# Performance work log

Measured on AMD Instinct MI355X. Metric: run time of the kernel, lower is better.

## Reference

```python
import jax, jax.numpy as jnp
import numpy as np

T, A = 768, 24          # tokens, dense atoms per token
S, Q, K = 576, 32, 128  # subsets, queries per subset, keys per subset
C, H, DH, L = 128, 4, 32, 3  # c_query, heads, head dim, transformer blocks
PAIR, PTC, FF = 16, 384, 256


def _ln(x, s, b):
    m = jnp.mean(x, axis=-1, keepdims=True)
    v = jnp.var(x, axis=-1, keepdims=True)
    return (x - m) * jax.lax.rsqrt(v + 1e-5) * s + b


def _convert(idxs, mask, arr):
    # atom_layout.convertV2: flatten the two layout axes, gather, apply mask
    flat = arr.reshape(-1, arr.shape[-1])
    return flat[idxs] * mask[..., None].astype(arr.dtype)


def setup_inputs() -> dict:
    key = jax.random.key(0)
    ks = jax.random.split(key, 32)
    sc = 0.02
    inp = {
        'queries_mask': jax.random.randint(ks[0], (S, Q), 0, 2, dtype=jnp.int32),
        'pred_dense_atom_mask': jax.random.randint(ks[1], (T, A), 0, 2, dtype=jnp.int32),
        'acat_atoms_to_q_gather_idxs': jax.random.randint(ks[2], (S, Q), 0, T * A, dtype=jnp.int32),
        'acat_atoms_to_q_gather_mask': jax.random.randint(ks[3], (S, Q), 0, 2, dtype=jnp.int32),
        'acat_q_to_k_gather_idxs': jax.random.randint(ks[4], (S, K), 0, S * Q, dtype=jnp.int32),
        'acat_q_to_k_gather_mask': jax.random.randint(ks[5], (S, K), 0, 2, dtype=jnp.int32),
        'acat_q_to_atom_gather_idxs': jax.random.randint(ks[6], (T, A), 0, S * Q, dtype=jnp.int32),
        'acat_q_to_atom_gather_mask': jax.random.randint(ks[7], (T, A), 0, 2, dtype=jnp.int32),
        'token_atoms_act': jax.random.normal(ks[8], (T, A, 3), dtype=jnp.float32),
        'queries_single_cond': jax.random.normal(ks[9], (S, Q, C), dtype=jnp.float32),
        'pair_act': jax.random.normal(ks[10], (S, Q, K, PAIR), dtype=jnp.float32),
        'keys_mask': jax.random.randint(ks[11], (S, K), 0, 2, dtype=jnp.int32),
        'keys_single_cond': jax.random.normal(ks[12], (S, K, C), dtype=jnp.float32),
        # learned params
        'w_pos': jax.random.normal(ks[13], (3, C), dtype=jnp.float32) * sc,
        'w_aggr': jax.random.normal(ks[14], (C, PTC), dtype=jnp.float32) * sc,
        'ln1_s': jnp.ones((L, C), jnp.float32),
        'ln1_b': jnp.zeros((L, C), jnp.float32),
        'wq': jax.random.normal(ks[15], (L, C, H, DH), dtype=jnp.float32) * sc,
        'wk': jax.random.normal(ks[16], (L, C, H, DH), dtype=jnp.float32) * sc,
        'wv': jax.random.normal(ks[17], (L, C, H, DH), dtype=jnp.float32) * sc,
        'wpair': jax.random.normal(ks[18], (L, PAIR, H), dtype=jnp.float32) * sc,
        'wo': jax.random.normal(ks[19], (L, H, DH, C), dtype=jnp.float32) * sc,
        'ln2_s': jnp.ones((L, C), jnp.float32),
        'ln2_b': jnp.zeros((L, C), jnp.float32),
        'w1': jax.random.normal(ks[20], (L, C, FF), dtype=jnp.float32) * sc,
        'w2': jax.random.normal(ks[21], (L, FF, C), dtype=jnp.float32) * sc,
    }
    return inp


def reference(queries_mask, pred_dense_atom_mask, acat_atoms_to_q_gather_idxs,
              acat_atoms_to_q_gather_mask, acat_q_to_k_gather_idxs, acat_q_to_k_gather_mask,
              acat_q_to_atom_gather_idxs, acat_q_to_atom_gather_mask, token_atoms_act,
              queries_single_cond, pair_act, keys_mask, keys_single_cond,
              w_pos, w_aggr, ln1_s, ln1_b, wq, wk, wv, wpair, wo, ln2_s, ln2_b, w1, w2):
    qm = queries_mask.astype(jnp.float32)
    km = keys_mask.astype(jnp.float32)
    # gather token atoms into queries layout, project positions to features
    x = _convert(acat_atoms_to_q_gather_idxs, acat_atoms_to_q_gather_mask, token_atoms_act)
    x = x @ w_pos                      # (S,Q,C)
    x = x * qm[..., None]
    x = x + queries_single_cond
    # DiffusionCrossAttTransformer: L blocks of cross-attn with pair bias
    for l in range(L):
        xn = _ln(x, ln1_s[l], ln1_b[l])
        keys_act = _convert(acat_q_to_k_gather_idxs, acat_q_to_k_gather_mask, xn) + keys_single_cond
        q = jnp.einsum('sqc,chd->sqhd', xn, wq[l]) * (DH ** -0.5)
        k = jnp.einsum('skc,chd->skhd', keys_act, wk[l])
        v = jnp.einsum('skc,chd->skhd', keys_act, wv[l])
        bias = jnp.einsum('sqkp,ph->sqkh', pair_act, wpair[l])
        logits = jnp.einsum('sqhd,skhd->sqkh', q, k) + bias + (km[:, None, :, None] - 1.0) * 1e9
        attn = jax.nn.softmax(logits, axis=2)
        x = x + jnp.einsum('sqkh,skhd,hdc->sqc', attn, v, wo[l])
        xn2 = _ln(x, ln2_s[l], ln2_b[l])
        x = x + jax.nn.relu(xn2 @ w1[l]) @ w2[l]
    x = x * qm[..., None]
    skip_connection = x
    proj = x @ w_aggr                  # (S,Q,PTC)
    tok_atoms = _convert(acat_q_to_atom_gather_idxs, acat_q_to_atom_gather_mask, proj)  # (T,A,PTC)
    m = pred_dense_atom_mask.astype(jnp.float32)[..., None]
    token_act = jnp.sum(m * jax.nn.relu(tok_atoms), axis=-2) / (jnp.sum(m, axis=-2) + 1e-10)
    return (token_act, skip_connection)
```

## Files before the change

kernel.cpp:

```cpp
#include <hip/hip_runtime.h>
#include <hip/hip_bf16.h>

#define T_ 768
#define A_ 24
#define S_ 576
#define Q_ 32
#define K_ 128
#define C_ 128
#define H_ 4
#define DH_ 32
#define L_ 3
#define PAIR_ 16
#define PTC_ 384
#define FF_ 256
#define SQ_ (S_*Q_)
#define SK_ (S_*K_)

typedef __attribute__((ext_vector_type(8))) short bf16x8;
typedef __attribute__((ext_vector_type(4))) short bf16x4;
typedef __attribute__((ext_vector_type(4))) float f32x4;
typedef unsigned short ushort_t;

#define MFMA(a,b,c) __builtin_amdgcn_mfma_f32_16x16x32_bf16(a,b,c,0,0,0)

__device__ inline unsigned short f2b(float f) {
    union { float f; unsigned u; } v; v.f = f;
    unsigned u = v.u;
    return (unsigned short)((u + 0x7FFFu + ((u >> 16) & 1u)) >> 16);
}
__device__ inline float b2f(unsigned short b) {
    union { unsigned u; float f; } v; v.u = ((unsigned)b) << 16;
    return v.f;
}
__device__ inline float dot4(float4 a, float4 b) {
    return a.x*b.x + a.y*b.y + a.z*b.z + a.w*b.w;
}

template<int KD>
__device__ inline bf16x8 ldfrag(const unsigned short* lds, int row, int k) {
    int byte = ((row*KD + k)*2) ^ ((row & 7) << 4);
    return *(const bf16x8*)((const char*)lds + byte);
}

__device__ inline void ln_rows64(const float* __restrict__ x, size_t r0,
                                 const float* __restrict__ s, const float* __restrict__ b,
                                 unsigned short* at, ushort_t* __restrict__ xn16_opt) {
    int t = threadIdx.x;
    int row = t >> 2, q = t & 3;
    size_t gr = r0 + row;
    float v[32];
    const float4* xp = (const float4*)(x + gr*C_ + q*32);
    #pragma unroll
    for (int i = 0; i < 8; i++) {
        float4 f = xp[i];
        v[i*4]=f.x; v[i*4+1]=f.y; v[i*4+2]=f.z; v[i*4+3]=f.w;
    }
    float sum = 0.f;
    #pragma unroll
    for (int i = 0; i < 32; i++) sum += v[i];
    sum += __shfl_xor(sum, 1); sum += __shfl_xor(sum, 2);
    float mean = sum * (1.0f/C_);
    float sq = 0.f;
    #pragma unroll
    for (int i = 0; i < 32; i++) { float d = v[i]-mean; sq += d*d; }
    sq += __shfl_xor(sq, 1); sq += __shfl_xor(sq, 2);
    float rs = rsqrtf(sq * (1.0f/C_) + 1e-5f);
    #pragma unroll
    for (int i8 = 0; i8 < 4; i8++) {
        int c0 = q*32 + i8*8;
        const float4* sp = (const float4*)(s + c0);
        const float4* bp = (const float4*)(b + c0);
        float4 s0 = sp[0], s1 = sp[1], b0 = bp[0], b1 = bp[1];
        bf16x8 o;
        o[0] = (short)f2b((v[i8*8+0]-mean)*rs*s0.x + b0.x);
        o[1] = (short)f2b((v[i8*8+1]-mean)*rs*s0.y + b0.y);
        o[2] = (short)f2b((v[i8*8+2]-mean)*rs*s0.z + b0.z);
        o[3] = (short)f2b((v[i8*8+3]-mean)*rs*s0.w + b0.w);
        o[4] = (short)f2b((v[i8*8+4]-mean)*rs*s1.x + b1.x);
        o[5] = (short)f2b((v[i8*8+5]-mean)*rs*s1.y + b1.y);
        o[6] = (short)f2b((v[i8*8+6]-mean)*rs*s1.z + b1.z);
        o[7] = (short)f2b((v[i8*8+7]-mean)*rs*s1.w + b1.w);
        int byte = ((row*C_ + c0)*2) ^ ((row & 7) << 4);
        *(bf16x8*)((char*)at + byte) = o;
        if (xn16_opt) *(bf16x8*)(xn16_opt + gr*C_ + c0) = o;
    }
}

__device__ inline void wtr(const float* __restrict__ src, ushort_t* __restrict__ dst,
                           int e, int KD, int ND) {
    int l = e / (KD*ND), r = e % (KD*ND);
    int n = r / KD, k = r % KD;
    dst[e] = f2b(src[(size_t)l*KD*ND + (size_t)k*ND + n]);
}

#define NB_WPREP ((4*L_*C_*C_ + 2*L_*C_*FF_ + C_*PTC_)/256)
#define NB_INIT  ((SQ_*C_)/256)
#define NB_KSC   ((SK_*C_)/1024)

__global__ __launch_bounds__(256) void k_bias(const float* __restrict__ pair,
                                              const float* __restrict__ wpair,
                                              ushort_t* __restrict__ bias16) {
    __shared__ float wp[L_*H_][PAIR_];
    int t = threadIdx.x;
    if (t < L_*H_*PAIR_) {
        int lh = t >> 4, p = t & 15;
        wp[lh][p] = wpair[(lh>>2)*PAIR_*H_ + p*H_ + (lh&3)];
    }
    __syncthreads();
    int s = blockIdx.x >> 3, qg = blockIdx.x & 7;
    int qq = qg*4 + (t >> 6);
    int kk0 = (t & 63)*2;
    const float4* pp = (const float4*)(pair + (((size_t)s*Q_ + qq)*K_ + kk0)*PAIR_);
    float4 pa0 = pp[0], pa1 = pp[1], pa2 = pp[2], pa3 = pp[3];
    float4 pb0 = pp[4], pb1 = pp[5], pb2 = pp[6], pb3 = pp[7];
    #pragma unroll
    for (int lh = 0; lh < L_*H_; lh++) {
        const float4* w4 = (const float4*)&wp[lh][0];
        float4 w0 = w4[0], w1 = w4[1], w2 = w4[2], w3 = w4[3];
        float a = dot4(pa0,w0) + dot4(pa1,w1) + dot4(pa2,w2) + dot4(pa3,w3);
        float b = dot4(pb0,w0) + dot4(pb1,w1) + dot4(pb2,w2) + dot4(pb3,w3);
        unsigned pack = (unsigned)f2b(a) | ((unsigned)f2b(b) << 16);
        int l = lh >> 2, h = lh & 3;
        *(unsigned*)(bias16 + (((size_t)l*S_ + s)*H_ + h)*(Q_*K_) + qq*K_ + kk0) = pack;
    }
}

__global__ __launch_bounds__(256) void k_prep(
    const float* __restrict__ wq, const float* __restrict__ wk, const float* __restrict__ wv,
    const float* __restrict__ w1, const float* __restrict__ w2, const float* __restrict__ wo,
    const float* __restrict__ w_aggr,
    ushort_t* __restrict__ wqT, ushort_t* __restrict__ wkT, ushort_t* __restrict__ wvT,
    ushort_t* __restrict__ w1T, ushort_t* __restrict__ w2T, ushort_t* __restrict__ woT,
    ushort_t* __restrict__ waT,
    const int* __restrict__ a2q_idx, const int* __restrict__ a2q_mask,
    const int* __restrict__ qmask, const float* __restrict__ ta_act,
    const float* __restrict__ qsc, const float* __restrict__ w_pos, float* __restrict__ x,
    const float* __restrict__ ksc, ushort_t* __restrict__ ksc16) {
    int blk = blockIdx.x, t = threadIdx.x;
    if (blk < NB_WPREP) {
        int e = blk * 256 + t;
        const int s_cc = L_*C_*C_;
        const int s_cf = L_*C_*FF_;
        if (e < s_cc)      { wtr(wq, wqT, e, C_, C_); return; }
        e -= s_cc;
        if (e < s_cc)      { wtr(wk, wkT, e, C_, C_); return; }
        e -= s_cc;
        if (e < s_cc)      { wtr(wv, wvT, e, C_, C_); return; }
        e -= s_cc;
        if (e < s_cf)      { wtr(w1, w1T, e, C_, FF_); return; }
        e -= s_cf;
        if (e < s_cf)      { wtr(w2, w2T, e, FF_, C_); return; }
        e -= s_cf;
        if (e < s_cc)      { wtr(wo, woT, e, C_, C_); return; }
        e -= s_cc;
        wtr(w_aggr, waT, e, C_, PTC_);
        return;
    }
    blk -= NB_WPREP;
    if (blk < NB_INIT) {
        int i = blk * 256 + t;
        int r = i / C_, c = i % C_;
        float v = 0.f;
        if (a2q_mask[r]) {
            int idx = a2q_idx[r];
            float p0 = ta_act[idx*3+0], p1 = ta_act[idx*3+1], p2 = ta_act[idx*3+2];
            v = p0 * w_pos[c] + p1 * w_pos[C_+c] + p2 * w_pos[2*C_+c];
        }
        v *= (float)qmask[r];
        x[i] = v + qsc[i];
        return;
    }
    blk -= NB_INIT;
    {
        int e4 = blk * 256 + t;
        float4 f = ((const float4*)ksc)[e4];
        bf16x4 o;
        o[0] = (short)f2b(f.x); o[1] = (short)f2b(f.y);
        o[2] = (short)f2b(f.z); o[3] = (short)f2b(f.w);
        *(bf16x4*)(ksc16 + (size_t)e4*4) = o;
    }
}

__global__ __launch_bounds__(256) void k_lnqproj(const float* __restrict__ x,
                                                 const float* __restrict__ s, const float* __restrict__ b,
                                                 const ushort_t* __restrict__ wqT,
                                                 ushort_t* __restrict__ xn16,
                                                 ushort_t* __restrict__ qb16) {
    __shared__ unsigned short at[64*C_];
    size_t r0 = (size_t)blockIdx.x * 64;
    ln_rows64(x, r0, s, b, at, xn16);
    __syncthreads();
    int t = threadIdx.x, wid = t>>6, lane = t&63, lr = lane&15, g = lane>>4;
    int mh = (wid&1)*32, nh = (wid>>1)*64;
    f32x4 acc[2][4] = {};
    #pragma unroll
    for (int ks = 0; ks < 4; ks++) {
        int ka = ks*32 + g*8;
        bf16x8 a0 = ldfrag<C_>(at, mh + lr, ka);
        bf16x8 a1 = ldfrag<C_>(at, mh + 16 + lr, ka);
        #pragma unroll
        for (int nt = 0; nt < 4; nt++) {
            bf16x8 bb = *(const bf16x8*)(wqT + (size_t)(nh + nt*16 + lr)*C_ + ka);
            acc[0][nt] = MFMA(a0, bb, acc[0][nt]);
            acc[1][nt] = MFMA(a1, bb, acc[1][nt]);
        }
    }
    const float scale = 0.17677669529663687f;
    #pragma unroll
    for (int mt = 0; mt < 2; mt++)
    #pragma unroll
    for (int nt = 0; nt < 4; nt++)
    #pragma unroll
    for (int r = 0; r < 4; r++) {
        int row = (int)r0 + mh + mt*16 + g*4 + r;
        int col = nh + nt*16 + lr;
        int s2 = row>>5, qq = row&31, h = col>>5, dd = col&31;
        qb16[(((size_t)s2*H_ + h)*Q_ + qq)*DH_ + dd] = f2b(acc[mt][nt][r] * scale);
    }
}

__global__ __launch_bounds__(256) void k_kv_m(const ushort_t* __restrict__ xn16,
    const int* __restrict__ q2k_idx, const int* __restrict__ q2k_mask,
    const ushort_t* __restrict__ ksc16,
    const ushort_t* __restrict__ wkT, const ushort_t* __restrict__ wvT,
    ushort_t* __restrict__ kb16, ushort_t* __restrict__ vT16) {
    __shared__ unsigned short at[64*C_];
    int t = threadIdx.x, wid = t>>6, lane = t&63, lr = lane&15, g = lane>>4;
    int r0 = blockIdx.x * 64;
    for (int e8 = t; e8 < 64*(C_/8); e8 += 256) {
        int row = e8 >> 4, c8 = (e8 & 15)*8;
        int gr = r0 + row;
        bf16x8 kc8 = *(const bf16x8*)(ksc16 + (size_t)gr*C_ + c8);
        bf16x8 o;
        if (q2k_mask[gr]) {
            bf16x8 xv = *(const bf16x8*)(xn16 + (size_t)q2k_idx[gr]*C_ + c8);
            #pragma unroll
            for (int j = 0; j < 8; j++)
                o[j] = (short)f2b(b2f((unsigned short)xv[j]) + b2f((unsigned short)kc8[j]));
        } else {
            o = kc8;
        }
        int byte = ((row*C_ + c8)*2) ^ ((row & 7) << 4);
        *(bf16x8*)((char*)at + byte) = o;
    }
    __syncthreads();
    int mh = (wid&1)*32, nh = (wid>>1)*64;
    f32x4 acc[2][4][2] = {};
    #pragma unroll
    for (int ks = 0; ks < 4; ks++) {
        int ka = ks*32 + g*8;
        bf16x8 a0 = ldfrag<C_>(at, mh + lr, ka);
        bf16x8 a1 = ldfrag<C_>(at, mh + 16 + lr, ka);
        #pragma unroll
        for (int nt = 0; nt < 4; nt++) {
            bf16x8 bk = *(const bf16x8*)(wkT + (size_t)(nh + nt*16 + lr)*C_ + ka);
            bf16x8 bv = *(const bf16x8*)(wvT + (size_t)(nh + nt*16 + lr)*C_ + ka);
            acc[0][nt][0] = MFMA(a0, bk, acc[0][nt][0]);
            acc[1][nt][0] = MFMA(a1, bk, acc[1][nt][0]);
            acc[0][nt][1] = MFMA(a0, bv, acc[0][nt][1]);
            acc[1][nt][1] = MFMA(a1, bv, acc[1][nt][1]);
        }
    }
    #pragma unroll
    for (int mt = 0; mt < 2; mt++)
    #pragma unroll
    for (int nt = 0; nt < 4; nt++)
    #pragma unroll
    for (int r = 0; r < 4; r++) {
        int row = r0 + mh + mt*16 + g*4 + r;
        int col = nh + nt*16 + lr;
        int s = row>>7, kk = row&127, h = col>>5, dd = col&31;
        kb16[(((size_t)s*H_ + h)*K_ + kk)*DH_ + dd] = f2b(acc[mt][nt][0][r]);
        vT16[(((size_t)s*H_ + h)*DH_ + dd)*K_ + kk] = f2b(acc[mt][nt][1][r]);
    }
}

__global__ __launch_bounds__(256) void k_mega(
    const ushort_t* __restrict__ qb16_in, const ushort_t* __restrict__ kb16,
    const ushort_t* __restrict__ vT16, const ushort_t* __restrict__ bias16,
    const int* __restrict__ kmask_g, const ushort_t* __restrict__ woT16,
    float* __restrict__ x,
    const float* __restrict__ ln2_s, const float* __restrict__ ln2_b,
    const ushort_t* __restrict__ w1T, const ushort_t* __restrict__ w2T,
    const float* __restrict__ ln1_s, const float* __restrict__ ln1_b,
    const ushort_t* __restrict__ wqT_next,
    ushort_t* __restrict__ xn16, ushort_t* __restrict__ qb16_out,
    const int* __restrict__ qmask_opt, float* __restrict__ skip_opt) {
    __shared__ __align__(16) char smem[40960];
    unsigned short* BP    = (unsigned short*)smem;
    unsigned short* O_lds = (unsigned short*)(smem + 32768);
    unsigned short* at    = (unsigned short*)smem;
    unsigned short* fft   = (unsigned short*)(smem + 8192);
    float*          stats = (float*)(smem + 32768);

    int s = blockIdx.x, t = threadIdx.x;
    int w = t>>6, lane = t&63, lr = lane&15, g = lane>>4;

    {
        const ushort_t* bb = bias16 + (size_t)s*H_*Q_*K_;
        for (int e8 = t; e8 < H_*Q_*K_/8; e8 += 256) {
            int h = e8 >> 9, rem = e8 & 511;
            int qq = rem >> 4, kk0 = (rem & 15)*8;
            bf16x8 v = *(const bf16x8*)(bb + h*(Q_*K_) + qq*K_ + kk0);
            int byte = ((qq*K_ + kk0)*2) ^ (((qq>>2)&3)<<5);
            *(bf16x8*)((char*)(BP + h*(Q_*K_)) + byte) = v;
        }
    }

    const ushort_t* qbase = qb16_in + ((size_t)(s*H_ + w)*Q_)*DH_;
    bf16x8 aq0 = *(const bf16x8*)(qbase + (size_t)lr*DH_ + g*8);
    bf16x8 aq1 = *(const bf16x8*)(qbase + (size_t)(16+lr)*DH_ + g*8);

    const ushort_t* kbase = kb16 + ((size_t)(s*H_ + w)*K_)*DH_;
    f32x4 acc[2][8] = {};
    #pragma unroll
    for (int nt = 0; nt < 8; nt++) {
        bf16x8 b = *(const bf16x8*)(kbase + (size_t)(nt*16+lr)*DH_ + g*8);
        acc[0][nt] = MFMA(aq0, b, acc[0][nt]);
        acc[1][nt] = MFMA(aq1, b, acc[1][nt]);
    }

    float km[8];
    #pragma unroll
    for (int nt = 0; nt < 8; nt++) km[nt] = (kmask_g[s*K_ + nt*16 + lr] - 1.0f) * 1e9f;

    __syncthreads();

    unsigned short* Pb = BP + w*(Q_*K_);
    #pragma unroll
    for (int mt = 0; mt < 2; mt++)
    #pragma unroll
    for (int r = 0; r < 4; r++) {
        int qq = mt*16 + g*4 + r;
        #pragma unroll
        for (int nt = 0; nt < 8; nt++) {
            int byte = ((qq*K_ + nt*16 + lr)*2) ^ (((qq>>2)&3)<<5);
            acc[mt][nt][r] += b2f(*(unsigned short*)((char*)Pb + byte)) + km[nt];
        }
    }

    float inv[2][4];
    #pragma unroll
    for (int mt = 0; mt < 2; mt++)
    #pragma unroll
    for (int r = 0; r < 4; r++) {
        float mx = acc[mt][0][r];
        #pragma unroll
        for (int nt = 1; nt < 8; nt++) mx = fmaxf(mx, acc[mt][nt][r]);
        #pragma unroll
        for (int m = 1; m <= 8; m <<= 1) mx = fmaxf(mx, __shfl_xor(mx, m));
        float sum = 0.f;
        #pragma unroll
        for (int nt = 0; nt < 8; nt++) {
            float e = __expf(acc[mt][nt][r] - mx);
            acc[mt][nt][r] = e;
            sum += e;
        }
        #pragma unroll
        for (int m = 1; m <= 8; m <<= 1) sum += __shfl_xor(sum, m);
        inv[mt][r] = 1.0f / sum;
    }

    #pragma unroll
    for (int mt = 0; mt < 2; mt++)
    #pragma unroll
    for (int r = 0; r < 4; r++) {
        int row = mt*16 + g*4 + r;
        #pragma unroll
        for (int nt = 0; nt < 8; nt++) {
            int byte = ((row*K_ + nt*16 + lr)*2) ^ ((row & 7) << 4);
            *(unsigned short*)((char*)Pb + byte) = f2b(acc[mt][nt][r]);
        }
    }

    const ushort_t* vbase = vT16 + ((size_t)(s*H_ + w)*DH_)*K_;
    f32x4 po[2][2] = {};
    #pragma unroll
    for (int ks = 0; ks < 4; ks++) {
        int kk0 = ks*32 + g*8;
        bf16x8 a0 = ldfrag<K_>(Pb, lr, kk0);
        bf16x8 a1 = ldfrag<K_>(Pb, 16 + lr, kk0);
        #pragma unroll
        for (int nt = 0; nt < 2; nt++) {
            bf16x8 b = *(const bf16x8*)(vbase + (size_t)(nt*16+lr)*K_ + kk0);
            po[0][nt] = MFMA(a0, b, po[0][nt]);
            po[1][nt] = MFMA(a1, b, po[1][nt]);
        }
    }

    #pragma unroll
    for (int mt = 0; mt < 2; mt++)
    #pragma unroll
    for (int nt = 0; nt < 2; nt++)
    #pragma unroll
    for (int r = 0; r < 4; r++) {
        int row = mt*16 + g*4 + r;
        int col = w*32 + nt*16 + lr;
        int byte = ((row*C_ + col)*2) ^ ((row & 7) << 4);
        *(unsigned short*)((char*)O_lds + byte) = f2b(po[mt][nt][r] * inv[mt][r]);
    }
    __syncthreads();

    f32x4 fo[2][2] = {};
    #pragma unroll
    for (int ks = 0; ks < 4; ks++) {
        int k0 = ks*32 + g*8;
        bf16x8 a0 = ldfrag<C_>(O_lds, lr, k0);
        bf16x8 a1 = ldfrag<C_>(O_lds, 16 + lr, k0);
        #pragma unroll
        for (int nt = 0; nt < 2; nt++) {
            bf16x8 b = *(const bf16x8*)(woT16 + (size_t)(w*32 + nt*16 + lr)*C_ + k0);
            fo[0][nt] = MFMA(a0, b, fo[0][nt]);
            fo[1][nt] = MFMA(a1, b, fo[1][nt]);
        }
    }

    float xres[2][2][4];
    #pragma unroll
    for (int mt = 0; mt < 2; mt++)
    #pragma unroll
    for (int nt = 0; nt < 2; nt++)
    #pragma unroll
    for (int r = 0; r < 4; r++) {
        int row = mt*16 + g*4 + r;
        int col = w*32 + nt*16 + lr;
        xres[mt][nt][r] = x[((size_t)s*Q_ + row)*C_ + col] + fo[mt][nt][r];
    }
    __syncthreads();

    int col0 = w*32 + lr, col1 = w*32 + 16 + lr;

    {
        float ps[2][4], pq[2][4];
        #pragma unroll
        for (int mt = 0; mt < 2; mt++)
        #pragma unroll
        for (int r = 0; r < 4; r++) {
            float a = xres[mt][0][r], b = xres[mt][1][r];
            float sum = a + b, sq = a*a + b*b;
            #pragma unroll
            for (int m = 1; m <= 8; m <<= 1) { sum += __shfl_xor(sum, m); sq += __shfl_xor(sq, m); }
            ps[mt][r] = sum; pq[mt][r] = sq;
        }
        if (lr == 0) {
            #pragma unroll
            for (int mt = 0; mt < 2; mt++)
            #pragma unroll
            for (int r = 0; r < 4; r++) {
                int row = mt*16 + g*4 + r;
                stats[row*8 + w*2]     = ps[mt][r];
                stats[row*8 + w*2 + 1] = pq[mt][r];
            }
        }
        __syncthreads();
        float lnsc0 = ln2_s[col0], lnsc1 = ln2_s[col1];
        float lnbb0 = ln2_b[col0], lnbb1 = ln2_b[col1];
        #pragma unroll
        for (int mt = 0; mt < 2; mt++)
        #pragma unroll
        for (int r = 0; r < 4; r++) {
            int row = mt*16 + g*4 + r;
            float sm = stats[row*8+0] + stats[row*8+2] + stats[row*8+4] + stats[row*8+6];
            float sq = stats[row*8+1] + stats[row*8+3] + stats[row*8+5] + stats[row*8+7];
            float mean = sm * (1.0f/C_);
            float var = sq * (1.0f/C_) - mean*mean;
            float rs = rsqrtf(var + 1e-5f);
            float xn0 = (xres[mt][0][r] - mean) * rs * lnsc0 + lnbb0;
            float xn1 = (xres[mt][1][r] - mean) * rs * lnsc1 + lnbb1;
            int b0 = ((row*C_ + col0)*2) ^ ((row & 7) << 4);
            int b1 = ((row*C_ + col1)*2) ^ ((row & 7) << 4);
            *(unsigned short*)((char*)at + b0) = f2b(xn0);
            *(unsigned short*)((char*)at + b1) = f2b(xn1);
        }
    }
    __syncthreads();

    {
        int nh = w*64;
        f32x4 acc1[2][4] = {};
        #pragma unroll
        for (int ks = 0; ks < 4; ks++) {
            int ka = ks*32 + g*8;
            bf16x8 a0 = ldfrag<C_>(at, lr, ka);
            bf16x8 a1 = ldfrag<C_>(at, 16 + lr, ka);
            #pragma unroll
            for (int nt = 0; nt < 4; nt++) {
                bf16x8 bb = *(const bf16x8*)(w1T + (size_t)(nh + nt*16 + lr)*C_ + ka);
                acc1[0][nt] = MFMA(a0, bb, acc1[0][nt]);
                acc1[1][nt] = MFMA(a1, bb, acc1[1][nt]);
            }
        }
        __syncthreads();
        #pragma unroll
        for (int mt = 0; mt < 2; mt++)
        #pragma unroll
        for (int nt = 0; nt < 4; nt++)
        #pragma unroll
        for (int r = 0; r < 4; r++) {
            int row = mt*16 + g*4 + r;
            int col = nh + nt*16 + lr;
            int byte = ((row*FF_ + col)*2) ^ ((row & 7) << 4);
            *(unsigned short*)((char*)fft + byte) = f2b(fmaxf(acc1[mt][nt][r], 0.f));
        }
    }
    __syncthreads();

    {
        int nq = w*32;
        f32x4 acc2[2][2] = {};
        #pragma unroll
        for (int ks = 0; ks < 8; ks++) {
            int ka = ks*32 + g*8;
            bf16x8 a0 = ldfrag<FF_>(fft, lr, ka);
            bf16x8 a1 = ldfrag<FF_>(fft, 16 + lr, ka);
            #pragma unroll
            for (int nt = 0; nt < 2; nt++) {
                bf16x8 bb = *(const bf16x8*)(w2T + (size_t)(nq + nt*16 + lr)*FF_ + ka);
                acc2[0][nt] = MFMA(a0, bb, acc2[0][nt]);
                acc2[1][nt] = MFMA(a1, bb, acc2[1][nt]);
            }
        }
        #pragma unroll
        for (int mt = 0; mt < 2; mt++)
        #pragma unroll
        for (int nt = 0; nt < 2; nt++)
        #pragma unroll
        for (int r = 0; r < 4; r++) {
            int row = mt*16 + g*4 + r;
            int col = nq + nt*16 + lr;
            size_t o = ((size_t)s*Q_ + row)*C_ + col;
            float v2 = xres[mt][nt][r] + acc2[mt][nt][r];
            if (qmask_opt) {
                v2 *= (float)qmask_opt[s*Q_ + row];
                skip_opt[o] = v2;
            }
            x[o] = v2;
            xres[mt][nt][r] = v2;
        }
    }
    if (!wqT_next) return;
    __syncthreads();

    {
        float ps[2][4], pq[2][4];
        #pragma unroll
        for (int mt = 0; mt < 2; mt++)
        #pragma unroll
        for (int r = 0; r < 4; r++) {
            float a = xres[mt][0][r], b = xres[mt][1][r];
            float sum = a + b, sq = a*a + b*b;
            #pragma unroll
            for (int m = 1; m <= 8; m <<= 1) { sum += __shfl_xor(sum, m); sq += __shfl_xor(sq, m); }
            ps[mt][r] = sum; pq[mt][r] = sq;
        }
        if (lr == 0) {
            #pragma unroll
            for (int mt = 0; mt < 2; mt++)
            #pragma unroll
            for (int r = 0; r < 4; r++) {
                int row = mt*16 + g*4 + r;
                stats[row*8 + w*2]     = ps[mt][r];
                stats[row*8 + w*2 + 1] = pq[mt][r];
            }
        }
        __syncthreads();
        float lnsc0 = ln1_s[col0], lnsc1 = ln1_s[col1];
        float lnbb0 = ln1_b[col0], lnbb1 = ln1_b[col1];
        #pragma unroll
        for (int mt = 0; mt < 2; mt++)
        #pragma unroll
        for (int r = 0; r < 4; r++) {
            int row = mt*16 + g*4 + r;
            float sm = stats[row*8+0] + stats[row*8+2] + stats[row*8+4] + stats[row*8+6];
            float sq = stats[row*8+1] + stats[row*8+3] + stats[row*8+5] + stats[row*8+7];
            float mean = sm * (1.0f/C_);
            float var = sq * (1.0f/C_) - mean*mean;
            float rs = rsqrtf(var + 1e-5f);
            float xn0 = (xres[mt][0][r] - mean) * rs * lnsc0 + lnbb0;
            float xn1 = (xres[mt][1][r] - mean) * rs * lnsc1 + lnbb1;
            unsigned short h0 = f2b(xn0), h1 = f2b(xn1);
            int b0 = ((row*C_ + col0)*2) ^ ((row & 7) << 4);
            int b1 = ((row*C_ + col1)*2) ^ ((row & 7) << 4);
            *(unsigned short*)((char*)at + b0) = h0;
            *(unsigned short*)((char*)at + b1) = h1;
            size_t gro = ((size_t)s*Q_ + row)*C_;
            xn16[gro + col0] = h0;
            xn16[gro + col1] = h1;
        }
    }
    __syncthreads();

    {
        f32x4 acc3[2][2] = {};
        #pragma unroll
        for (int ks = 0; ks < 4; ks++) {
            int ka = ks*32 + g*8;
            bf16x8 a0 = ldfrag<C_>(at, lr, ka);
            bf16x8 a1 = ldfrag<C_>(at, 16 + lr, ka);
            #pragma unroll
            for (int nt = 0; nt < 2; nt++) {
                bf16x8 bb = *(const bf16x8*)(wqT_next + (size_t)(w*32 + nt*16 + lr)*C_ + ka);
                acc3[0][nt] = MFMA(a0, bb, acc3[0][nt]);
                acc3[1][nt] = MFMA(a1, bb, acc3[1][nt]);
            }
        }
        const float scale = 0.17677669529663687f;
        #pragma unroll
        for (int mt = 0; mt < 2; mt++)
        #pragma unroll
        for (int nt = 0; nt < 2; nt++)
        #pragma unroll
        for (int r = 0; r < 4; r++) {
            int row = mt*16 + g*4 + r;
            int dd = nt*16 + lr;
            qb16_out[(((size_t)s*H_ + w)*Q_ + row)*DH_ + dd] = f2b(acc3[mt][nt][r] * scale);
        }
    }
}

__global__ __launch_bounds__(256) void k_token_m(const float* __restrict__ x,
                                                 const int* __restrict__ q2a_idx,
                                                 const int* __restrict__ q2a_mask,
                                                 const int* __restrict__ dmask,
                                                 const ushort_t* __restrict__ waT,
                                                 float* __restrict__ out) {
    __shared__ unsigned short xs[32*C_];
    __shared__ float am[32];
    int tt = blockIdx.x, t = threadIdx.x;
    int w = t>>6, lane = t&63, lr = lane&15, g = lane>>4;

    for (int e8 = t; e8 < 32*(C_/8); e8 += 256) {
        int row = e8 >> 4, c8 = (e8 & 15)*8;
        bf16x8 o = {};
        if (row < A_) {
            int gm = q2a_mask[tt*A_ + row];
            if (gm) {
                const float4* xp = (const float4*)(x + (size_t)q2a_idx[tt*A_ + row]*C_ + c8);
                float4 f0 = xp[0], f1 = xp[1];
                o[0]=(short)f2b(f0.x); o[1]=(short)f2b(f0.y); o[2]=(short)f2b(f0.z); o[3]=(short)f2b(f0.w);
                o[4]=(short)f2b(f1.x); o[5]=(short)f2b(f1.y); o[6]=(short)f2b(f1.z); o[7]=(short)f2b(f1.w);
            }
        }
        int byte = ((row*C_ + c8)*2) ^ ((row & 7) << 4);
        *(bf16x8*)((char*)xs + byte) = o;
    }
    if (t < 32) am[t] = (t < A_) ? (float)dmask[tt*A_ + t] : 0.f;
    __syncthreads();

    f32x4 acc[2][6] = {};
    #pragma unroll
    for (int ks = 0; ks < 4; ks++) {
        int ka = ks*32 + g*8;
        bf16x8 a0 = ldfrag<C_>(xs, lr, ka);
        bf16x8 a1 = ldfrag<C_>(xs, 16 + lr, ka);
        #pragma unroll
        for (int nt = 0; nt < 6; nt++) {
            bf16x8 b = *(const bf16x8*)(waT + (size_t)(w*96 + nt*16 + lr)*C_ + ka);
            acc[0][nt] = MFMA(a0, b, acc[0][nt]);
            acc[1][nt] = MFMA(a1, b, acc[1][nt]);
        }
    }

    float amr[2][4];
    #pragma unroll
    for (int mt = 0; mt < 2; mt++)
    #pragma unroll
    for (int r = 0; r < 4; r++) amr[mt][r] = am[mt*16 + g*4 + r];
    float denom = 1e-10f;
    #pragma unroll
    for (int a = 0; a < A_; a++) denom += am[a];
    float invd = 1.0f / denom;
    #pragma unroll
    for (int nt = 0; nt < 6; nt++) {
        float v = 0.f;
        #pragma unroll
        for (int mt = 0; mt < 2; mt++)
        #pragma unroll
        for (int r = 0; r < 4; r++) v += amr[mt][r] * fmaxf(acc[mt][nt][r], 0.f);
        v += __shfl_xor(v, 16);
        v += __shfl_xor(v, 32);
        if (g == 0) out[(size_t)tt*PTC_ + w*96 + nt*16 + lr] = v * invd;
    }
}

extern "C" void kernel_launch(void* const* d_in, const int* in_sizes, int n_in,
                              void* d_out, int out_size, void* d_ws, size_t ws_size,
                              hipStream_t stream) {
    const int*   qmask    = (const int*)d_in[0];
    const int*   dmask    = (const int*)d_in[1];
    const int*   a2q_idx  = (const int*)d_in[2];
    const int*   a2q_mask = (const int*)d_in[3];
    const int*   q2k_idx  = (const int*)d_in[4];
    const int*   q2k_mask = (const int*)d_in[5];
    const int*   q2a_idx  = (const int*)d_in[6];
    const int*   q2a_mask = (const int*)d_in[7];
    const float* ta_act   = (const float*)d_in[8];
    const float* qsc      = (const float*)d_in[9];
    const float* pair     = (const float*)d_in[10];
    const int*   kmask    = (const int*)d_in[11];
    const float* ksc      = (const float*)d_in[12];
    const float* w_pos    = (const float*)d_in[13];
    const float* w_aggr   = (const float*)d_in[14];
    const float* ln1_s    = (const float*)d_in[15];
    const float* ln1_b    = (const float*)d_in[16];
    const float* wq       = (const float*)d_in[17];
    const float* wk       = (const float*)d_in[18];
    const float* wv       = (const float*)d_in[19];
    const float* wpair    = (const float*)d_in[20];
    const float* wo       = (const float*)d_in[21];
    const float* ln2_s    = (const float*)d_in[22];
    const float* ln2_b    = (const float*)d_in[23];
    const float* w1       = (const float*)d_in[24];
    const float* w2       = (const float*)d_in[25];
    float* out = (float*)d_out;

    float* ws = (float*)d_ws;
    float*    x      = ws;
    ushort_t* xn16   = (ushort_t*)(x + (size_t)SQ_*C_);
    ushort_t* qb16   = xn16 + (size_t)SQ_*C_;
    ushort_t* kb16   = qb16 + (size_t)SQ_*C_;
    ushort_t* vT16   = kb16 + (size_t)S_*H_*K_*DH_;
    ushort_t* bias16 = vT16 + (size_t)S_*H_*K_*DH_;
    ushort_t* woT16  = bias16 + (size_t)L_*S_*H_*Q_*K_;
    ushort_t* wqT16  = woT16 + (size_t)L_*C_*C_;
    ushort_t* wkT16  = wqT16 + (size_t)L_*C_*C_;
    ushort_t* wvT16  = wkT16 + (size_t)L_*C_*C_;
    ushort_t* w1T16  = wvT16 + (size_t)L_*C_*C_;
    ushort_t* w2T16  = w1T16 + (size_t)L_*C_*FF_;
    ushort_t* waT16  = w2T16 + (size_t)L_*FF_*C_;
    ushort_t* ksc16  = waT16 + (size_t)PTC_*C_;

    k_prep<<<NB_WPREP + NB_INIT + NB_KSC, 256, 0, stream>>>(
        wq, wk, wv, w1, w2, wo, w_aggr,
        wqT16, wkT16, wvT16, w1T16, w2T16, woT16, waT16,
        a2q_idx, a2q_mask, qmask, ta_act, qsc, w_pos, x,
        ksc, ksc16);
    k_bias<<<S_*8, 256, 0, stream>>>(pair, wpair, bias16);
    k_lnqproj<<<SQ_/64, 256, 0, stream>>>(x, ln1_s, ln1_b, wqT16, xn16, qb16);

    for (int l = 0; l < L_; l++) {
        k_kv_m<<<SK_/64, 256, 0, stream>>>(xn16, q2k_idx, q2k_mask, ksc16,
                                           wkT16 + (size_t)l*C_*C_, wvT16 + (size_t)l*C_*C_,
                                           kb16, vT16);
        int last = (l == L_-1);
        k_mega<<<S_, 256, 0, stream>>>(qb16, kb16, vT16,
                                       bias16 + (size_t)l*S_*H_*Q_*K_, kmask,
                                       woT16 + (size_t)l*C_*C_, x,
                                       ln2_s + l*C_, ln2_b + l*C_,
                                       w1T16 + (size_t)l*C_*FF_, w2T16 + (size_t)l*FF_*C_,
                                       last ? nullptr : (ln1_s + (l+1)*C_),
                                       last ? nullptr : (ln1_b + (l+1)*C_),
                                       last ? nullptr : (wqT16 + (size_t)(l+1)*C_*C_),
                                       xn16, qb16,
                                       last ? qmask : nullptr,
                                       last ? (out + (size_t)T_*PTC_) : nullptr);
    }

    k_token_m<<<T_, 256, 0, stream>>>(x, q2a_idx, q2a_mask, dmask, waT16, out);
}
```

Baseline: 328.9 us.

## Split k_mega work across 8 waves by head and query-row half

Doubles the k_mega block size from 256 to 512 threads. Each wave now handles one head and one 16-row half of the queries instead of a whole head, and the FFN first-layer columns are split across 8 waves. The goal is more wave parallelism per block, since there are only 576 blocks on a large GPU, plus fewer registers per thread. The cost is that K, V and weight fragments are loaded twice (once per half) and more threads take part in each barrier.

Measured after the change: 334.6 us. Within noise of the previous version (+1.7%).

```diff
diff --git a/kernel.cpp b/kernel.cpp
--- a/kernel.cpp
+++ b/kernel.cpp
@@ -275,7 +275,7 @@
     }
 }
 
-__global__ __launch_bounds__(256) void k_mega(
+__global__ __launch_bounds__(512) void k_mega(
     const ushort_t* __restrict__ qb16_in, const ushort_t* __restrict__ kb16,
     const ushort_t* __restrict__ vT16, const ushort_t* __restrict__ bias16,
     const int* __restrict__ kmask_g, const ushort_t* __restrict__ woT16,
@@ -294,11 +294,13 @@
     float*          stats = (float*)(smem + 32768);
 
     int s = blockIdx.x, t = threadIdx.x;
-    int w = t>>6, lane = t&63, lr = lane&15, g = lane>>4;
+    int w8 = t>>6, lane = t&63, lr = lane&15, g = lane>>4;
+    int hq = w8>>1, half = w8&1;
+    int rowbase = half*16;
 
     {
         const ushort_t* bb = bias16 + (size_t)s*H_*Q_*K_;
-        for (int e8 = t; e8 < H_*Q_*K_/8; e8 += 256) {
+        for (int e8 = t; e8 < H_*Q_*K_/8; e8 += 512) {
             int h = e8 >> 9, rem = e8 & 511;
             int qq = rem >> 4, kk0 = (rem & 15)*8;
             bf16x8 v = *(const bf16x8*)(bb + h*(Q_*K_) + qq*K_ + kk0);
@@ -307,17 +309,15 @@
         }
     }
 
-    const ushort_t* qbase = qb16_in + ((size_t)(s*H_ + w)*Q_)*DH_;
-    bf16x8 aq0 = *(const bf16x8*)(qbase + (size_t)lr*DH_ + g*8);
-    bf16x8 aq1 = *(const bf16x8*)(qbase + (size_t)(16+lr)*DH_ + g*8);
-
-    const ushort_t* kbase = kb16 + ((size_t)(s*H_ + w)*K_)*DH_;
-    f32x4 acc[2][8] = {};
+    const ushort_t* qbase = qb16_in + ((size_t)(s*H_ + hq)*Q_)*DH_;
+    bf16x8 aq = *(const bf16x8*)(qbase + (size_t)(rowbase + lr)*DH_ + g*8);
+
+    const ushort_t* kbase = kb16 + ((size_t)(s*H_ + hq)*K_)*DH_;
+    f32x4 acc[8] = {};
     #pragma unroll
     for (int nt = 0; nt < 8; nt++) {
         bf16x8 b = *(const bf16x8*)(kbase + (size_t)(nt*16+lr)*DH_ + g*8);
-        acc[0][nt] = MFMA(aq0, b, acc[0][nt]);
-        acc[1][nt] = MFMA(aq1, b, acc[1][nt]);
+        acc[nt] = MFMA(aq, b, acc[nt]);
     }
 
     float km[8];
@@ -326,147 +326,127 @@
 
     __syncthreads();
 
-    unsigned short* Pb = BP + w*(Q_*K_);
-    #pragma unroll
-    for (int mt = 0; mt < 2; mt++)
+    unsigned short* Pb = BP + hq*(Q_*K_);
     #pragma unroll
     for (int r = 0; r < 4; r++) {
-        int qq = mt*16 + g*4 + r;
+        int qq = rowbase + g*4 + r;
         #pragma unroll
         for (int nt = 0; nt < 8; nt++) {
             int byte = ((qq*K_ + nt*16 + lr)*2) ^ (((qq>>2)&3)<<5);
-            acc[mt][nt][r] += b2f(*(unsigned short*)((char*)Pb + byte)) + km[nt];
-        }
-    }
-
-    float inv[2][4];
-    #pragma unroll
-    for (int mt = 0; mt < 2; mt++)
+            acc[nt][r] += b2f(*(unsigned short*)((char*)Pb + byte)) + km[nt];
+        }
+    }
+
+    float inv[4];
     #pragma unroll
     for (int r = 0; r < 4; r++) {
-        float mx = acc[mt][0][r];
-        #pragma unroll
-        for (int nt = 1; nt < 8; nt++) mx = fmaxf(mx, acc[mt][nt][r]);
+        float mx = acc[0][r];
+        #pragma unroll
+        for (int nt = 1; nt < 8; nt++) mx = fmaxf(mx, acc[nt][r]);
         #pragma unroll
         for (int m = 1; m <= 8; m <<= 1) mx = fmaxf(mx, __shfl_xor(mx, m));
         float sum = 0.f;
         #pragma unroll
         for (int nt = 0; nt < 8; nt++) {
-            float e = __expf(acc[mt][nt][r] - mx);
-            acc[mt][nt][r] = e;
+            float e = __expf(acc[nt][r] - mx);
+            acc[nt][r] = e;
             sum += e;
         }
         #pragma unroll
         for (int m = 1; m <= 8; m <<= 1) sum += __shfl_xor(sum, m);
-        inv[mt][r] = 1.0f / sum;
-    }
-
-    #pragma unroll
-    for (int mt = 0; mt < 2; mt++)
+        inv[r] = 1.0f / sum;
+    }
+
     #pragma unroll
     for (int r = 0; r < 4; r++) {
-        int row = mt*16 + g*4 + r;
+        int row = rowbase + g*4 + r;
         #pragma unroll
         for (int nt = 0; nt < 8; nt++) {
             int byte = ((row*K_ + nt*16 + lr)*2) ^ ((row & 7) << 4);
-            *(unsigned short*)((char*)Pb + byte) = f2b(acc[mt][nt][r]);
-        }
-    }
-
-    const ushort_t* vbase = vT16 + ((size_t)(s*H_ + w)*DH_)*K_;
-    f32x4 po[2][2] = {};
+            *(unsigned short*)((char*)Pb + byte) = f2b(acc[nt][r]);
+        }
+    }
+
+    const ushort_t* vbase = vT16 + ((size_t)(s*H_ + hq)*DH_)*K_;
+    f32x4 po[2] = {};
     #pragma unroll
     for (int ks = 0; ks < 4; ks++) {
         int kk0 = ks*32 + g*8;
-        bf16x8 a0 = ldfrag<K_>(Pb, lr, kk0);
-        bf16x8 a1 = ldfrag<K_>(Pb, 16 + lr, kk0);
+        bf16x8 a = ldfrag<K_>(Pb, rowbase + lr, kk0);
         #pragma unroll
         for (int nt = 0; nt < 2; nt++) {
             bf16x8 b = *(const bf16x8*)(vbase + (size_t)(nt*16+lr)*K_ + kk0);
-            po[0][nt] = MFMA(a0, b, po[0][nt]);
-            po[1][nt] = MFMA(a1, b, po[1][nt]);
-        }
-    }
-
-    #pragma unroll
-    for (int mt = 0; mt < 2; mt++)
+            po[nt] = MFMA(a, b, po[nt]);
+        }
+    }
+
     #pragma unroll
     for (int nt = 0; nt < 2; nt++)
     #pragma unroll
     for (int r = 0; r < 4; r++) {
-        int row = mt*16 + g*4 + r;
-        int col = w*32 + nt*16 + lr;
+        int row = rowbase + g*4 + r;
+        int col = hq*32 + nt*16 + lr;
         int byte = ((row*C_ + col)*2) ^ ((row & 7) << 4);
-        *(unsigned short*)((char*)O_lds + byte) = f2b(po[mt][nt][r] * inv[mt][r]);
-    }
-    __syncthreads();
-
-    f32x4 fo[2][2] = {};
+        *(unsigned short*)((char*)O_lds + byte) = f2b(po[nt][r] * inv[r]);
+    }
+    __syncthreads();
+
+    f32x4 fo[2] = {};
     #pragma unroll
     for (int ks = 0; ks < 4; ks++) {
         int k0 = ks*32 + g*8;
-        bf16x8 a0 = ldfrag<C_>(O_lds, lr, k0);
-        bf16x8 a1 = ldfrag<C_>(O_lds, 16 + lr, k0);
+        bf16x8 a = ldfrag<C_>(O_lds, rowbase + lr, k0);
         #pragma unroll
         for (int nt = 0; nt < 2; nt++) {
-            bf16x8 b = *(const bf16x8*)(woT16 + (size_t)(w*32 + nt*16 + lr)*C_ + k0);
-            fo[0][nt] = MFMA(a0, b, fo[0][nt]);
-            fo[1][nt] = MFMA(a1, b, fo[1][nt]);
-        }
-    }
-
-    float xres[2][2][4];
-    #pragma unroll
-    for (int mt = 0; mt < 2; mt++)
+            bf16x8 b = *(const bf16x8*)(woT16 + (size_t)(hq*32 + nt*16 + lr)*C_ + k0);
+            fo[nt] = MFMA(a, b, fo[nt]);
+        }
+    }
+
+    float xres[2][4];
     #pragma unroll
     for (int nt = 0; nt < 2; nt++)
     #pragma unroll
     for (int r = 0; r < 4; r++) {
-        int row = mt*16 + g*4 + r;
-        int col = w*32 + nt*16 + lr;
-        xres[mt][nt][r] = x[((size_t)s*Q_ + row)*C_ + col] + fo[mt][nt][r];
-    }
-    __syncthreads();
-
-    int col0 = w*32 + lr, col1 = w*32 + 16 + lr;
+        int row = rowbase + g*4 + r;
+        int col = hq*32 + nt*16 + lr;
+        xres[nt][r] = x[((size_t)s*Q_ + row)*C_ + col] + fo[nt][r];
+    }
+    __syncthreads();
+
+    int col0 = hq*32 + lr, col1 = hq*32 + 16 + lr;
 
     {
-        float ps[2][4], pq[2][4];
-        #pragma unroll
-        for (int mt = 0; mt < 2; mt++)
+        float ps[4], pq[4];
         #pragma unroll
         for (int r = 0; r < 4; r++) {
-            float a = xres[mt][0][r], b = xres[mt][1][r];
+            float a = xres[0][r], b = xres[1][r];
             float sum = a + b, sq = a*a + b*b;
             #pragma unroll
             for (int m = 1; m <= 8; m <<= 1) { sum += __shfl_xor(sum, m); sq += __shfl_xor(sq, m); }
-            ps[mt][r] = sum; pq[mt][r] = sq;
+            ps[r] = sum; pq[r] = sq;
         }
         if (lr == 0) {
             #pragma unroll
-            for (int mt = 0; mt < 2; mt++)
-            #pragma unroll
             for (int r = 0; r < 4; r++) {
-                int row = mt*16 + g*4 + r;
-                stats[row*8 + w*2]     = ps[mt][r];
-                stats[row*8 + w*2 + 1] = pq[mt][r];
+                int row = rowbase + g*4 + r;
+                stats[row*8 + hq*2]     = ps[r];
+                stats[row*8 + hq*2 + 1] = pq[r];
             }
         }
         __syncthreads();
         float lnsc0 = ln2_s[col0], lnsc1 = ln2_s[col1];
         float lnbb0 = ln2_b[col0], lnbb1 = ln2_b[col1];
         #pragma unroll
-        for (int mt = 0; mt < 2; mt++)
-        #pragma unroll
         for (int r = 0; r < 4; r++) {
-            int row = mt*16 + g*4 + r;
+            int row = rowbase + g*4 + r;
             float sm = stats[row*8+0] + stats[row*8+2] + stats[row*8+4] + stats[row*8+6];
             float sq = stats[row*8+1] + stats[row*8+3] + stats[row*8+5] + stats[row*8+7];
             float mean = sm * (1.0f/C_);
             float var = sq * (1.0f/C_) - mean*mean;
             float rs = rsqrtf(var + 1e-5f);
-            float xn0 = (xres[mt][0][r] - mean) * rs * lnsc0 + lnbb0;
-            float xn1 = (xres[mt][1][r] - mean) * rs * lnsc1 + lnbb1;
+            float xn0 = (xres[0][r] - mean) * rs * lnsc0 + lnbb0;
+            float xn1 = (xres[1][r] - mean) * rs * lnsc1 + lnbb1;
             int b0 = ((row*C_ + col0)*2) ^ ((row & 7) << 4);
             int b1 = ((row*C_ + col1)*2) ^ ((row & 7) << 4);
             *(unsigned short*)((char*)at + b0) = f2b(xn0);
@@ -476,15 +456,15 @@
     __syncthreads();
 
     {
-        int nh = w*64;
-        f32x4 acc1[2][4] = {};
+        int nh = w8*32;
+        f32x4 acc1[2][2] = {};
         #pragma unroll
         for (int ks = 0; ks < 4; ks++) {
             int ka = ks*32 + g*8;
             bf16x8 a0 = ldfrag<C_>(at, lr, ka);
             bf16x8 a1 = ldfrag<C_>(at, 16 + lr, ka);
             #pragma unroll
-            for (int nt = 0; nt < 4; nt++) {
+            for (int nt = 0; nt < 2; nt++) {
                 bf16x8 bb = *(const bf16x8*)(w1T + (size_t)(nh + nt*16 + lr)*C_ + ka);
                 acc1[0][nt] = MFMA(a0, bb, acc1[0][nt]);
                 acc1[1][nt] = MFMA(a1, bb, acc1[1][nt]);
@@ -494,7 +474,7 @@
         #pragma unroll
         for (int mt = 0; mt < 2; mt++)
         #pragma unroll
-        for (int nt = 0; nt < 4; nt++)
+        for (int nt = 0; nt < 2; nt++)
         #pragma unroll
         for (int r = 0; r < 4; r++) {
             int row = mt*16 + g*4 + r;
@@ -506,78 +486,68 @@
     __syncthreads();
 
     {
-        int nq = w*32;
-        f32x4 acc2[2][2] = {};
+        int nq = hq*32;
+        f32x4 acc2[2] = {};
         #pragma unroll
         for (int ks = 0; ks < 8; ks++) {
             int ka = ks*32 + g*8;
-            bf16x8 a0 = ldfrag<FF_>(fft, lr, ka);
-            bf16x8 a1 = ldfrag<FF_>(fft, 16 + lr, ka);
+            bf16x8 a = ldfrag<FF_>(fft, rowbase + lr, ka);
             #pragma unroll
             for (int nt = 0; nt < 2; nt++) {
                 bf16x8 bb = *(const bf16x8*)(w2T + (size_t)(nq + nt*16 + lr)*FF_ + ka);
-                acc2[0][nt] = MFMA(a0, bb, acc2[0][nt]);
-                acc2[1][nt] = MFMA(a1, bb, acc2[1][nt]);
+                acc2[nt] = MFMA(a, bb, acc2[nt]);
             }
         }
         #pragma unroll
-        for (int mt = 0; mt < 2; mt++)
-        #pragma unroll
         for (int nt = 0; nt < 2; nt++)
         #pragma unroll
         for (int r = 0; r < 4; r++) {
-            int row = mt*16 + g*4 + r;
+            int row = rowbase + g*4 + r;
             int col = nq + nt*16 + lr;
             size_t o = ((size_t)s*Q_ + row)*C_ + col;
-            float v2 = xres[mt][nt][r] + acc2[mt][nt][r];
+            float v2 = xres[nt][r] + acc2[nt][r];
             if (qmask_opt) {
                 v2 *= (float)qmask_opt[s*Q_ + row];
                 skip_opt[o] = v2;
             }
             x[o] = v2;
-            xres[mt][nt][r] = v2;
+            xres[nt][r] = v2;
         }
     }
     if (!wqT_next) return;
     __syncthreads();
 
     {
-        float ps[2][4], pq[2][4];
-        #pragma unroll
-        for (int mt = 0; mt < 2; mt++)
+        float ps[4], pq[4];
         #pragma unroll
         for (int r = 0; r < 4; r++) {
-            float a = xres[mt][0][r], b = xres[mt][1][r];
+            float a = xres[0][r], b = xres[1][r];
             float sum = a + b, sq = a*a + b*b;
             #pragma unroll
             for (int m = 1; m <= 8; m <<= 1) { sum += __shfl_xor(sum, m); sq += __shfl_xor(sq, m); }
-            ps[mt][r] = sum; pq[mt][r] = sq;
+            ps[r] = sum; pq[r] = sq;
         }
         if (lr == 0) {
             #pragma unroll
-            for (int mt = 0; mt < 2; mt++)
-            #pragma unroll
             for (int r = 0; r < 4; r++) {
-                int row = mt*16 + g*4 + r;
-                stats[row*8 + w*2]     = ps[mt][r];
-                stats[row*8 + w*2 + 1] = pq[mt][r];
+                int row = rowbase + g*4 + r;
+                stats[row*8 + hq*2]     = ps[r];
+                stats[row*8 + hq*2 + 1] = pq[r];
             }
         }
         __syncthreads();
         float lnsc0 = ln1_s[col0], lnsc1 = ln1_s[col1];
         float lnbb0 = ln1_b[col0], lnbb1 = ln1_b[col1];
         #pragma unroll
-        for (int mt = 0; mt < 2; mt++)
-        #pragma unroll
         for (int r = 0; r < 4; r++) {
-            int row = mt*16 + g*4 + r;
+            int row = rowbase + g*4 + r;
             float sm = stats[row*8+0] + stats[row*8+2] + stats[row*8+4] + stats[row*8+6];
             float sq = stats[row*8+1] + stats[row*8+3] + stats[row*8+5] + stats[row*8+7];
             float mean = sm * (1.0f/C_);
             float var = sq * (1.0f/C_) - mean*mean;
             float rs = rsqrtf(var + 1e-5f);
-            float xn0 = (xres[mt][0][r] - mean) * rs * lnsc0 + lnbb0;
-            float xn1 = (xres[mt][1][r] - mean) * rs * lnsc1 + lnbb1;
+            float xn0 = (xres[0][r] - mean) * rs * lnsc0 + lnbb0;
+            float xn1 = (xres[1][r] - mean) * rs * lnsc1 + lnbb1;
             unsigned short h0 = f2b(xn0), h1 = f2b(xn1);
             int b0 = ((row*C_ + col0)*2) ^ ((row & 7) << 4);
             int b1 = ((row*C_ + col1)*2) ^ ((row & 7) << 4);
@@ -591,29 +561,25 @@
     __syncthreads();
 
     {
-        f32x4 acc3[2][2] = {};
+        f32x4 acc3[2] = {};
         #pragma unroll
         for (int ks = 0; ks < 4; ks++) {
             int ka = ks*32 + g*8;
-            bf16x8 a0 = ldfrag<C_>(at, lr, ka);
-            bf16x8 a1 = ldfrag<C_>(at, 16 + lr, ka);
+            bf16x8 a = ldfrag<C_>(at, rowbase + lr, ka);
             #pragma unroll
             for (int nt = 0; nt < 2; nt++) {
-                bf16x8 bb = *(const bf16x8*)(wqT_next + (size_t)(w*32 + nt*16 + lr)*C_ + ka);
-                acc3[0][nt] = MFMA(a0, bb, acc3[0][nt]);
-                acc3[1][nt] = MFMA(a1, bb, acc3[1][nt]);
+                bf16x8 bb = *(const bf16x8*)(wqT_next + (size_t)(hq*32 + nt*16 + lr)*C_ + ka);
+                acc3[nt] = MFMA(a, bb, acc3[nt]);
             }
         }
         const float scale = 0.17677669529663687f;
         #pragma unroll
-        for (int mt = 0; mt < 2; mt++)
-        #pragma unroll
         for (int nt = 0; nt < 2; nt++)
         #pragma unroll
         for (int r = 0; r < 4; r++) {
-            int row = mt*16 + g*4 + r;
+            int row = rowbase + g*4 + r;
             int dd = nt*16 + lr;
-            qb16_out[(((size_t)s*H_ + w)*Q_ + row)*DH_ + dd] = f2b(acc3[mt][nt][r] * scale);
+            qb16_out[(((size_t)s*H_ + hq)*Q_ + row)*DH_ + dd] = f2b(acc3[nt][r] * scale);
         }
     }
 }
@@ -743,7 +709,7 @@
                                            wkT16 + (size_t)l*C_*C_, wvT16 + (size_t)l*C_*C_,
                                            kb16, vT16);
         int last = (l == L_-1);
-        k_mega<<<S_, 256, 0, stream>>>(qb16, kb16, vT16,
+        k_mega<<<S_, 512, 0, stream>>>(qb16, kb16, vT16,
                                        bias16 + (size_t)l*S_*H_*Q_*K_, kmask,
                                        woT16 + (size_t)l*C_*C_, x,
                                        ln2_s + l*C_, ln2_b + l*C_,
```
